# Kernel optimization log

Hardware: AMD Instinct MI355X
Metric: run time of the kernel (lower is better)

## Reference

```python
import jax, jax.numpy as jnp
import numpy as np

HID = 1024   # hidden_size
HEADS = 16   # multi_head
DH = 64      # hidden_size_head
FF = 4096    # ff_size
EPS = 1e-6   # LayerNorm epsilon
NEG = -1e9


def setup_inputs() -> dict:
    key = jax.random.key(0)
    ks = jax.random.split(key, 24)
    B, LI, LQ, LK = 16, 512, 64, 128
    s = 0.02

    def w(k, shape):
        return jax.random.normal(k, shape, jnp.float32) * s

    return {
        "img_feat": jax.random.normal(ks[0], (B, LI, HID), jnp.float32),
        "ques": jax.random.normal(ks[1], (B, LQ, HID), jnp.float32),
        "kg": jax.random.normal(ks[2], (B, LK, HID), jnp.float32),
        "ques_mask": jax.random.randint(ks[3], (B, LQ), 0, 2, jnp.int32),
        "kg_mask": jax.random.randint(ks[4], (B, LK), 0, 2, jnp.int32),
        # stacked params for the 3 MHAtt blocks; torch Linear weight layout [out, in]
        "att_qw": w(ks[5], (3, HID, HID)), "att_qb": jnp.zeros((3, HID), jnp.float32),
        "att_kw": w(ks[6], (3, HID, HID)), "att_kb": jnp.zeros((3, HID), jnp.float32),
        "att_vw": w(ks[7], (3, HID, HID)), "att_vb": jnp.zeros((3, HID), jnp.float32),
        "att_ow": w(ks[8], (3, HID, HID)), "att_ob": jnp.zeros((3, HID), jnp.float32),
        "ffn_w1": w(ks[9], (FF, HID)), "ffn_b1": jnp.zeros((FF,), jnp.float32),
        "ffn_w2": w(ks[10], (HID, FF)), "ffn_b2": jnp.zeros((HID,), jnp.float32),
        "ln_g": jnp.ones((4, HID), jnp.float32), "ln_b": jnp.zeros((4, HID), jnp.float32),
    }


def _ln(x, g, b):
    m = jnp.mean(x, axis=-1, keepdims=True)
    v = jnp.mean(jnp.square(x - m), axis=-1, keepdims=True)
    return g * (x - m) / jnp.sqrt(v + EPS) + b


def _mha(v_in, k_in, q_in, mask, qw, qb, kw, kb, vw, vb, ow, ob):
    B = q_in.shape[0]

    def proj(x, wt, bi):  # [B,S,H] -> [B,heads,S,DH]
        y = jnp.einsum('bsh,oh->bso', x, wt) + bi
        return y.reshape(B, -1, HEADS, DH).transpose(0, 2, 1, 3)

    q = proj(q_in, qw, qb)
    k = proj(k_in, kw, kb)
    v = proj(v_in, vw, vb)
    scores = jnp.einsum('bhqd,bhkd->bhqk', q, k) / jnp.sqrt(jnp.float32(DH))
    if mask is not None:
        scores = jnp.where(mask[:, None, None, :] == 1, NEG, scores)
    a = jax.nn.softmax(scores, axis=-1)  # dropout is identity at eval
    o = jnp.einsum('bhqk,bhkd->bhqd', a, v).transpose(0, 2, 1, 3).reshape(B, -1, HID)
    return jnp.einsum('bsh,oh->bso', o, ow) + ob


def reference(img_feat, ques, kg, ques_mask, kg_mask,
              att_qw, att_qb, att_kw, att_kb, att_vw, att_vb, att_ow, att_ob,
              ffn_w1, ffn_b1, ffn_w2, ffn_b2, ln_g, ln_b):
    x = img_feat
    # self-attention on image features (no mask)
    x = _ln(x + _mha(x, x, x, None,
                     att_qw[0], att_qb[0], att_kw[0], att_kb[0],
                     att_vw[0], att_vb[0], att_ow[0], att_ob[0]), ln_g[0], ln_b[0])
    # cross-attention to question
    x = _ln(x + _mha(ques, ques, x, ques_mask,
                     att_qw[1], att_qb[1], att_kw[1], att_kb[1],
                     att_vw[1], att_vb[1], att_ow[1], att_ob[1]), ln_g[1], ln_b[1])
    # cross-attention to knowledge graph facts
    x = _ln(x + _mha(kg, kg, x, kg_mask,
                     att_qw[2], att_qb[2], att_kw[2], att_kb[2],
                     att_vw[2], att_vb[2], att_ow[2], att_ob[2]), ln_g[2], ln_b[2])
    # FFN: Linear -> ReLU -> Linear (dropout identity at eval)
    h = jax.nn.relu(jnp.einsum('bsh,fh->bsf', x, ffn_w1) + ffn_b1)
    f = jnp.einsum('bsf,hf->bsh', h, ffn_w2) + ffn_b2
    x = _ln(x + f, ln_g[3], ln_b[3])
    return x
```

## Files before the change

kernel.cpp:

```cpp
#include <hip/hip_runtime.h>
#include <math.h>

#define HIDN 1024
#define NHEADS 16
#define DHEAD 64
#define FFD 4096
#define LN_EPS 1e-6f
#define NEGV -1e9f

typedef __bf16 bf16_t;
typedef __bf16 bf16x8 __attribute__((ext_vector_type(8)));
typedef float f32x4 __attribute__((ext_vector_type(4)));
typedef unsigned short ushort8 __attribute__((ext_vector_type(8)));
typedef unsigned short ushort4v __attribute__((ext_vector_type(4)));

__device__ __forceinline__ unsigned short f2bf(float f) {
    unsigned u = __float_as_uint(f);
    return (unsigned short)((u + 0x7FFFu + ((u >> 16) & 1u)) >> 16);
}
__device__ __forceinline__ float bf2f(unsigned short u) {
    return __uint_as_float((unsigned)u << 16);
}
__device__ __forceinline__ void gld16(const void* g, void* l) {
    __builtin_amdgcn_global_load_lds(
        (const __attribute__((address_space(1))) void*)g,
        (__attribute__((address_space(3))) void*)l, 16, 0, 0);
}

template<int RELU>
__global__ __launch_bounds__(256)
void gemm_mfma(const bf16_t* __restrict__ A, const bf16_t* __restrict__ W,
               const float* __restrict__ ba, const float* __restrict__ bb,
               const float* __restrict__ bc, const float* __restrict__ bd,
               unsigned short* __restrict__ Cb, int M, int N, int K)
{
    __shared__ __align__(16) bf16_t As[2][128 * 64];
    __shared__ __align__(16) bf16_t Bs[2][128 * 64];

    const int tid  = threadIdx.x;
    const int wid  = tid >> 6;
    const int lane = tid & 63;
    const int m0 = blockIdx.x * 128;
    const int n0 = blockIdx.y * 128;
    const int wm = (wid & 1) * 64;
    const int wn = (wid >> 1) * 64;

    const int sr = (wid << 3) + (lane >> 3);
    const int sk = (((lane & 7) ^ (lane >> 3)) * 8);
    const bf16_t* pa = A + (size_t)(m0 + sr) * K + sk;
    const bf16_t* pb = W + (size_t)(n0 + sr) * K + sk;
    const int lofs = (wid << 3) * 64;

    const int lr  = lane & 15;
    const int hi_ = lane >> 4;
    const int ch0 = ((hi_ + 0) ^ (lane & 7)) * 8;
    const int ch1 = ((hi_ + 4) ^ (lane & 7)) * 8;

    f32x4 acc[4][4];
    #pragma unroll
    for (int i = 0; i < 4; ++i)
        #pragma unroll
        for (int j = 0; j < 4; ++j) acc[i][j] = (f32x4){0.f, 0.f, 0.f, 0.f};

    auto stage = [&](int buf, int koff) {
        #pragma unroll
        for (int c = 0; c < 4; ++c) {
            gld16(pa + (size_t)c * 32 * K + koff, &As[buf][lofs + c * 32 * 64]);
            gld16(pb + (size_t)c * 32 * K + koff, &Bs[buf][lofs + c * 32 * 64]);
        }
    };
    auto compute = [&](int buf) {
        const bf16_t* fa = &As[buf][(wm + lr) * 64];
        const bf16_t* fb = &Bs[buf][(wn + lr) * 64];
        #pragma unroll
        for (int kk = 0; kk < 2; ++kk) {
            const int ch = kk ? ch1 : ch0;
            bf16x8 a[4], b[4];
            #pragma unroll
            for (int i = 0; i < 4; ++i) {
                a[i] = *(const bf16x8*)(fa + i * 16 * 64 + ch);
                b[i] = *(const bf16x8*)(fb + i * 16 * 64 + ch);
            }
            #pragma unroll
            for (int i = 0; i < 4; ++i)
                #pragma unroll
                for (int j = 0; j < 4; ++j)
                    acc[i][j] = __builtin_amdgcn_mfma_f32_16x16x32_bf16(
                        a[i], b[j], acc[i][j], 0, 0, 0);
        }
    };

    stage(0, 0);
    asm volatile("s_waitcnt vmcnt(0)" ::: "memory");
    __syncthreads();

    for (int k0 = 0; k0 < K; k0 += 128) {
        if (k0 + 64 < K) stage(1, k0 + 64);
        compute(0);
        asm volatile("s_waitcnt vmcnt(0)" ::: "memory");
        __syncthreads();
        if (k0 + 128 < K) stage(0, k0 + 128);
        compute(1);
        asm volatile("s_waitcnt vmcnt(0)" ::: "memory");
        __syncthreads();
    }

    const int seg = n0 >> 10;
    const float* bias = (seg == 0) ? ba : (seg == 1) ? bb : (seg == 2) ? bc : bd;
    const int nl = (n0 & 1023);
    const int er = wm + (lane >> 4) * 4;
    const int ec = wn + (lane & 15);
    float bv[4];
    #pragma unroll
    for (int j = 0; j < 4; ++j) bv[j] = bias[nl + ec + j * 16];
    #pragma unroll
    for (int i = 0; i < 4; ++i)
        #pragma unroll
        for (int j = 0; j < 4; ++j)
            #pragma unroll
            for (int r = 0; r < 4; ++r) {
                float v = acc[i][j][r] + bv[j];
                if (RELU) v = fmaxf(v, 0.f);
                Cb[(size_t)(m0 + er + i * 16 + r) * N + (n0 + ec + j * 16)] = f2bf(v);
            }
}

#define MFMA16(F0, F1, F2, F3)                                                      \
    acc[F0][0] = __builtin_amdgcn_mfma_f32_16x16x32_bf16(a0, b0, acc[F0][0], 0,0,0); \
    acc[F0][1] = __builtin_amdgcn_mfma_f32_16x16x32_bf16(a0, b1, acc[F0][1], 0,0,0); \
    acc[F0][2] = __builtin_amdgcn_mfma_f32_16x16x32_bf16(a0, b2, acc[F0][2], 0,0,0); \
    acc[F0][3] = __builtin_amdgcn_mfma_f32_16x16x32_bf16(a0, b3, acc[F0][3], 0,0,0); \
    acc[F1][0] = __builtin_amdgcn_mfma_f32_16x16x32_bf16(a1, b0, acc[F1][0], 0,0,0); \
    acc[F1][1] = __builtin_amdgcn_mfma_f32_16x16x32_bf16(a1, b1, acc[F1][1], 0,0,0); \
    acc[F1][2] = __builtin_amdgcn_mfma_f32_16x16x32_bf16(a1, b2, acc[F1][2], 0,0,0); \
    acc[F1][3] = __builtin_amdgcn_mfma_f32_16x16x32_bf16(a1, b3, acc[F1][3], 0,0,0); \
    acc[F2][0] = __builtin_amdgcn_mfma_f32_16x16x32_bf16(a2, b0, acc[F2][0], 0,0,0); \
    acc[F2][1] = __builtin_amdgcn_mfma_f32_16x16x32_bf16(a2, b1, acc[F2][1], 0,0,0); \
    acc[F2][2] = __builtin_amdgcn_mfma_f32_16x16x32_bf16(a2, b2, acc[F2][2], 0,0,0); \
    acc[F2][3] = __builtin_amdgcn_mfma_f32_16x16x32_bf16(a2, b3, acc[F2][3], 0,0,0); \
    acc[F3][0] = __builtin_amdgcn_mfma_f32_16x16x32_bf16(a3, b0, acc[F3][0], 0,0,0); \
    acc[F3][1] = __builtin_amdgcn_mfma_f32_16x16x32_bf16(a3, b1, acc[F3][1], 0,0,0); \
    acc[F3][2] = __builtin_amdgcn_mfma_f32_16x16x32_bf16(a3, b2, acc[F3][2], 0,0,0); \
    acc[F3][3] = __builtin_amdgcn_mfma_f32_16x16x32_bf16(a3, b3, acc[F3][3], 0,0,0);

#define PHASE_SYNC()                                           \
    __builtin_amdgcn_s_barrier();                              \
    asm volatile("s_waitcnt lgkmcnt(0)" ::: "memory");         \
    __builtin_amdgcn_sched_barrier(0);

template<int RELU>
__global__ __launch_bounds__(512, 1)
void gemm_mfma256(const bf16_t* __restrict__ A, const bf16_t* __restrict__ W,
                  const float* __restrict__ ba, const float* __restrict__ bb,
                  const float* __restrict__ bc, const float* __restrict__ bd,
                  unsigned short* __restrict__ Cb, int M, int N, int K)
{
    __shared__ __align__(16) bf16_t As[2][256 * 64];
    __shared__ __align__(16) bf16_t Bs[2][256 * 64];

    const int tid  = threadIdx.x;
    const int wid  = tid >> 6;
    const int lane = tid & 63;
    const int lo   = lane & 15;
    const int hi   = lane >> 4;

    const int GY = gridDim.y;
    const int id = blockIdx.y * gridDim.x + blockIdx.x;
    const int xcd = id & 7;
    const int c   = id >> 3;
    const int CN  = GY >> 1;
    const int m_idx = ((xcd & 3) << 3) + (c & 7);
    const int n_idx = (xcd >> 2) * CN + (c >> 3);
    const int m0 = m_idx * 256;
    const int n0 = n_idx * 256;

    const int wm = (wid & 1) * 128;
    const int wn = (wid >> 1) * 64;

    const int srow = tid >> 3;
    const int ssk  = (((tid & 7) ^ (srow & 7)) * 8);
    const bf16_t* pa = A + (size_t)(m0 + srow) * K + ssk;
    const bf16_t* pb = W + (size_t)(n0 + srow) * K + ssk;
    const int lbase = (wid << 3) * 64;

    auto stageA = [&](int buf, int koff) {
        #pragma unroll
        for (int i = 0; i < 4; ++i)
            gld16(pa + (size_t)i * 64 * K + koff, &As[buf][i * 64 * 64 + lbase]);
    };
    auto stageB = [&](int buf, int koff) {
        #pragma unroll
        for (int i = 0; i < 4; ++i)
            gld16(pb + (size_t)i * 64 * K + koff, &Bs[buf][i * 64 * 64 + lbase]);
    };

    auto ldA = [&](int buf, int f, int cc) -> bf16x8 {
        const int row = wm + f * 16 + lo;
        const int ch  = ((cc * 4 + hi) ^ (lo & 7)) * 8;
        return *(const bf16x8*)&As[buf][row * 64 + ch];
    };
    auto ldB = [&](int buf, int g, int cc) -> bf16x8 {
        const int row = wn + g * 16 + lo;
        const int ch  = ((cc * 4 + hi) ^ (lo & 7)) * 8;
        return *(const bf16x8*)&Bs[buf][row * 64 + ch];
    };

    f32x4 acc[8][4];
    #pragma unroll
    for (int f = 0; f < 8; ++f)
        #pragma unroll
        for (int g = 0; g < 4; ++g) acc[f][g] = (f32x4){0.f, 0.f, 0.f, 0.f};

    stageA(0, 0);
    stageB(0, 0);
    asm volatile("s_waitcnt vmcnt(0)" ::: "memory");
    __builtin_amdgcn_s_barrier();

    const int nt = K >> 6;
    for (int t = 0; t < nt; ++t) {
        const int buf = t & 1;
        const int knext = (t + 1) << 6;
        const bool pf = (t + 1 < nt);
        bf16x8 a0, a1, a2, a3, b0, b1, b2, b3;

        a0 = ldA(buf, 0, 0); a1 = ldA(buf, 1, 0); a2 = ldA(buf, 2, 0); a3 = ldA(buf, 3, 0);
        b0 = ldB(buf, 0, 0); b1 = ldB(buf, 1, 0); b2 = ldB(buf, 2, 0); b3 = ldB(buf, 3, 0);
        if (pf) stageA(buf ^ 1, knext);
        PHASE_SYNC();
        __builtin_amdgcn_s_setprio(1);
        MFMA16(0, 1, 2, 3);
        __builtin_amdgcn_s_setprio(0);
        __builtin_amdgcn_s_barrier();

        a0 = ldA(buf, 4, 0); a1 = ldA(buf, 5, 0); a2 = ldA(buf, 6, 0); a3 = ldA(buf, 7, 0);
        if (pf) stageB(buf ^ 1, knext);
        PHASE_SYNC();
        __builtin_amdgcn_s_setprio(1);
        MFMA16(4, 5, 6, 7);
        __builtin_amdgcn_s_setprio(0);
        __builtin_amdgcn_s_barrier();

        a0 = ldA(buf, 0, 1); a1 = ldA(buf, 1, 1); a2 = ldA(buf, 2, 1); a3 = ldA(buf, 3, 1);
        b0 = ldB(buf, 0, 1); b1 = ldB(buf, 1, 1); b2 = ldB(buf, 2, 1); b3 = ldB(buf, 3, 1);
        PHASE_SYNC();
        __builtin_amdgcn_s_setprio(1);
        MFMA16(0, 1, 2, 3);
        __builtin_amdgcn_s_setprio(0);
        __builtin_amdgcn_s_barrier();

        a0 = ldA(buf, 4, 1); a1 = ldA(buf, 5, 1); a2 = ldA(buf, 6, 1); a3 = ldA(buf, 7, 1);
        PHASE_SYNC();
        __builtin_amdgcn_s_setprio(1);
        MFMA16(4, 5, 6, 7);
        __builtin_amdgcn_s_setprio(0);
        asm volatile("s_waitcnt vmcnt(0)" ::: "memory");
        __builtin_amdgcn_s_barrier();
    }

    const int seg = n0 >> 10;
    const float* bias = (seg == 0) ? ba : (seg == 1) ? bb : (seg == 2) ? bc : bd;
    const int nl = (n0 & 1023);
    float bv[4];
    #pragma unroll
    for (int g = 0; g < 4; ++g) bv[g] = bias[nl + wn + g * 16 + lo];
    #pragma unroll
    for (int f = 0; f < 8; ++f)
        #pragma unroll
        for (int g = 0; g < 4; ++g)
            #pragma unroll
            for (int r = 0; r < 4; ++r) {
                float v = acc[f][g][r] + bv[g];
                if (RELU) v = fmaxf(v, 0.f);
                Cb[(size_t)(m0 + wm + f * 16 + hi * 4 + r) * N
                   + (n0 + wn + g * 16 + lo)] = f2bf(v);
            }
}

template<int HAS_MASK>
__global__ __launch_bounds__(512, 2)
void attn_mfma(const bf16_t* __restrict__ Q, const bf16_t* __restrict__ K,
               const bf16_t* __restrict__ V, int qstride, int kvstride,
               const int* __restrict__ mask,
               unsigned short* __restrict__ O, int Lk)
{
    __shared__ __align__(16) unsigned short Ks[64][72];
    __shared__ __align__(16) unsigned short Vt[64][72];
    __shared__ __align__(16) unsigned short Ps[128][72];
    __shared__ int smask[64];

    const int tid  = threadIdx.x;
    const int wid  = tid >> 6;
    const int lane = tid & 63;
    const int lo   = lane & 15;
    const int hi   = lane >> 4;
    const int h    = blockIdx.x;
    const int b    = blockIdx.y;
    const int Lq   = 512;

    bf16x8 qf[4][2];
    #pragma unroll
    for (int s4 = 0; s4 < 4; ++s4) {
        const bf16_t* qp = Q + (size_t)(b*Lq + s4*128 + wid*16 + lo) * qstride
                             + h*DHEAD + hi*8;
        qf[s4][0] = *(const bf16x8*)qp;
        qf[s4][1] = *(const bf16x8*)(qp + 32);
    }

    float mrun[4][4], lrun[4][4];
    f32x4 Oc[4][4];
    #pragma unroll
    for (int s4 = 0; s4 < 4; ++s4)
        #pragma unroll
        for (int r = 0; r < 4; ++r) {
            mrun[s4][r] = -INFINITY; lrun[s4][r] = 0.f;
            Oc[s4][r] = (f32x4){0.f, 0.f, 0.f, 0.f};
        }

    ushort8 r0, r1;
    int mreg = 0;

    auto load_tile = [&](int k0) {
        if (tid < 256) {
            const int sr = tid >> 2, sc = (tid & 3) * 16;
            const unsigned short* kp = (const unsigned short*)
                (K + (size_t)(b*Lk + k0 + sr) * kvstride + h*DHEAD + sc);
            r0 = *(const ushort8*)kp;
            r1 = *(const ushort8*)(kp + 8);
        } else {
            const int t2 = tid - 256, sr = t2 >> 2, sc = (t2 & 3) * 16;
            const unsigned short* vp = (const unsigned short*)
                (V + (size_t)(b*Lk + k0 + sr) * kvstride + h*DHEAD + sc);
            r0 = *(const ushort8*)vp;
            r1 = *(const ushort8*)(vp + 8);
        }
        if (HAS_MASK && tid < 64) mreg = mask[b*Lk + k0 + tid];
    };
    auto store_tile = [&]() {
        if (tid < 256) {
            const int sr = tid >> 2, sc = (tid & 3) * 16;
            const int x = ((sr >> 3) & 7) << 3;
            *(ushort8*)&Ks[sr][sc ^ x]       = r0;
            *(ushort8*)&Ks[sr][(sc + 8) ^ x] = r1;
        } else {
            const int t2 = tid - 256, sr = t2 >> 2, sc = (t2 & 3) * 16;
            #pragma unroll
            for (int t = 0; t < 8; ++t) {
                const int d0 = sc + t, d1 = sc + 8 + t;
                Vt[d0][sr ^ (((d0 >> 3) & 7) << 3)] = r0[t];
                Vt[d1][sr ^ (((d1 >> 3) & 7) << 3)] = r1[t];
            }
        }
        if (HAS_MASK && tid < 64) smask[tid] = mreg;
    };

    load_tile(0);
    store_tile();
    __syncthreads();

    int k0 = 0;
    while (true) {
        const bool more = (k0 + 64 < Lk);
        if (more) load_tile(k0 + 64);

        #pragma unroll
        for (int s4 = 0; s4 < 4; ++s4) {
            f32x4 sv[4];
            #pragma unroll
            for (int j = 0; j < 4; ++j) sv[j] = (f32x4){0.f, 0.f, 0.f, 0.f};
            #pragma unroll
            for (int kk = 0; kk < 2; ++kk) {
                #pragma unroll
                for (int j = 0; j < 4; ++j) {
                    const int krow = j*16 + lo;
                    const int kcol = (kk*32 + hi*8) ^ (((krow >> 3) & 7) << 3);
                    bf16x8 bfrag = *(const bf16x8*)&Ks[krow][kcol];
                    sv[j] = __builtin_amdgcn_mfma_f32_16x16x32_bf16(
                        qf[s4][kk], bfrag, sv[j], 0, 0, 0);
                }
            }
            #pragma unroll
            for (int j = 0; j < 4; ++j) {
                bool msk = HAS_MASK ? (smask[j*16 + lo] != 0) : false;
                #pragma unroll
                for (int r = 0; r < 4; ++r) {
                    float x = sv[j][r] * 0.125f;
                    sv[j][r] = msk ? NEGV : x;
                }
            }
            #pragma unroll
            for (int r = 0; r < 4; ++r) {
                float tm = fmaxf(fmaxf(sv[0][r], sv[1][r]), fmaxf(sv[2][r], sv[3][r]));
                #pragma unroll
                for (int m = 1; m < 16; m <<= 1) tm = fmaxf(tm, __shfl_xor(tm, m));
                float mnew = fmaxf(mrun[s4][r], tm);
                float f = __expf(mrun[s4][r] - mnew);
                float ps = 0.f;
                #pragma unroll
                for (int j = 0; j < 4; ++j) {
                    float p = __expf(sv[j][r] - mnew);
                    sv[j][r] = p;
                    ps += p;
                }
                #pragma unroll
                for (int m = 1; m < 16; m <<= 1) ps += __shfl_xor(ps, m);
                lrun[s4][r] = lrun[s4][r] * f + ps;
                mrun[s4][r] = mnew;
                #pragma unroll
                for (int n = 0; n < 4; ++n) Oc[s4][n][r] *= f;
                #pragma unroll
                for (int j = 0; j < 4; ++j)
                    Ps[wid*16 + hi*4 + r][j*16 + lo] = f2bf(sv[j][r]);
            }
            #pragma unroll
            for (int kk = 0; kk < 2; ++kk) {
                bf16x8 pa = *(const bf16x8*)&Ps[wid*16 + lo][kk*32 + hi*8];
                #pragma unroll
                for (int n = 0; n < 4; ++n) {
                    const int vrow = n*16 + lo;
                    const int vcol = (kk*32 + hi*8) ^ (((vrow >> 3) & 7) << 3);
                    bf16x8 vf = *(const bf16x8*)&Vt[vrow][vcol];
                    Oc[s4][n] = __builtin_amdgcn_mfma_f32_16x16x32_bf16(
                        pa, vf, Oc[s4][n], 0, 0, 0);
                }
            }
        }

        if (!more) break;
        __syncthreads();
        store_tile();
        __syncthreads();
        k0 += 64;
    }

    #pragma unroll
    for (int s4 = 0; s4 < 4; ++s4)
        #pragma unroll
        for (int r = 0; r < 4; ++r) {
            float inv = 1.f / lrun[s4][r];
            const size_t row = (size_t)(b*Lq + s4*128 + wid*16 + hi*4 + r) * HIDN
                             + h*DHEAD;
            #pragma unroll
            for (int n = 0; n < 4; ++n)
                O[row + n*16 + lo] = f2bf(Oc[s4][n][r] * inv);
        }
}

template<int WF32, int WBF>
__global__ __launch_bounds__(256)
void ln_res_b(const unsigned short* __restrict__ X, const unsigned short* __restrict__ R,
              const float* __restrict__ G, const float* __restrict__ Bv,
              unsigned short* __restrict__ OutB, float* __restrict__ OutF)
{
    const int row = blockIdx.x;
    const int tid = threadIdx.x;
    const size_t base = (size_t)row * HIDN + tid * 4;
    ushort4v xv = *(const ushort4v*)(X + base);
    ushort4v rv = *(const ushort4v*)(R + base);
    float y[4];
    #pragma unroll
    for (int t = 0; t < 4; ++t) y[t] = bf2f(xv[t]) + bf2f(rv[t]);
    float s1 = y[0] + y[1] + y[2] + y[3];
    float s2 = y[0]*y[0] + y[1]*y[1] + y[2]*y[2] + y[3]*y[3];
    #pragma unroll
    for (int m = 1; m < 64; m <<= 1) {
        s1 += __shfl_xor(s1, m);
        s2 += __shfl_xor(s2, m);
    }
    __shared__ float red1[4], red2[4];
    const int wave = tid >> 6, lane = tid & 63;
    if (lane == 0) { red1[wave] = s1; red2[wave] = s2; }
    __syncthreads();
    s1 = red1[0] + red1[1] + red1[2] + red1[3];
    s2 = red2[0] + red2[1] + red2[2] + red2[3];
    const float mean = s1 * (1.f / HIDN);
    const float var  = s2 * (1.f / HIDN) - mean * mean;
    const float inv  = rsqrtf(var + LN_EPS);
    float4 gv = *(const float4*)(G + tid*4);
    float4 bv = *(const float4*)(Bv + tid*4);
    float o[4];
    o[0] = gv.x * (y[0]-mean) * inv + bv.x;
    o[1] = gv.y * (y[1]-mean) * inv + bv.y;
    o[2] = gv.z * (y[2]-mean) * inv + bv.z;
    o[3] = gv.w * (y[3]-mean) * inv + bv.w;
    if (WBF) {
        ushort4v ob;
        #pragma unroll
        for (int t = 0; t < 4; ++t) ob[t] = f2bf(o[t]);
        *(ushort4v*)(OutB + base) = ob;
    }
    if (WF32) {
        float4 of = {o[0], o[1], o[2], o[3]};
        *(float4*)(OutF + base) = of;
    }
}

struct CvtArgs {
    const float* src[32];
    unsigned short* dst[32];
};

__global__ __launch_bounds__(256)
void cvt_units(CvtArgs args)
{
    const float* s = args.src[blockIdx.y];
    unsigned short* d = args.dst[blockIdx.y];
    const int i = blockIdx.x * 256 + threadIdx.x;
    const float4* p = (const float4*)s + (size_t)i * 2;
    float4 a = p[0], b = p[1];
    ushort8 o;
    o[0] = f2bf(a.x); o[1] = f2bf(a.y); o[2] = f2bf(a.z); o[3] = f2bf(a.w);
    o[4] = f2bf(b.x); o[5] = f2bf(b.y); o[6] = f2bf(b.z); o[7] = f2bf(b.w);
    ((ushort8*)d)[i] = o;
}

extern "C" void kernel_launch(void* const* d_in, const int* in_sizes, int n_in,
                              void* d_out, int out_size, void* d_ws, size_t ws_size,
                              hipStream_t stream)
{
    const float* img   = (const float*)d_in[0];
    const float* ques  = (const float*)d_in[1];
    const float* kg    = (const float*)d_in[2];
    const int*   qmask = (const int*)d_in[3];
    const int*   kmask = (const int*)d_in[4];
    const float* qw = (const float*)d_in[5];
    const float* qb = (const float*)d_in[6];
    const float* kw = (const float*)d_in[7];
    const float* kb = (const float*)d_in[8];
    const float* vw = (const float*)d_in[9];
    const float* vb = (const float*)d_in[10];
    const float* ow = (const float*)d_in[11];
    const float* ob = (const float*)d_in[12];
    const float* w1 = (const float*)d_in[13];
    const float* b1 = (const float*)d_in[14];
    const float* w2 = (const float*)d_in[15];
    const float* b2 = (const float*)d_in[16];
    const float* lng = (const float*)d_in[17];
    const float* lnb = (const float*)d_in[18];
    float* out = (float*)d_out;

    const int B = 16;
    const int NX = B * 512;
    const size_t WSTEP = (size_t)1024 * 1024;
    const size_t MB = (size_t)1 << 20;
    const size_t MELEM = (size_t)1024 * 1024;

    char* wsb = (char*)d_ws;
    unsigned short* xb    = (unsigned short*)(wsb);
    unsigned short* bM    = (unsigned short*)(wsb + 16*MB);
    unsigned short* bOb   = (unsigned short*)(wsb + 32*MB);
    unsigned short* quesb = (unsigned short*)(wsb + 48*MB);
    unsigned short* kgb   = (unsigned short*)(wsb + 50*MB);
    unsigned short* wa    = (unsigned short*)(wsb + 56*MB);
    unsigned short* bQKV  = (unsigned short*)(wsb + 96*MB);
    unsigned short* bKV   = (unsigned short*)(wsb + 144*MB);
    unsigned short* hb    = (unsigned short*)(wsb + 96*MB);

    CvtArgs ca;
    int u = 0;
    auto addu = [&](const float* src, int melems, unsigned short* dst) {
        for (int i = 0; i < melems; ++i) {
            ca.src[u] = src + (size_t)i * MELEM;
            ca.dst[u] = dst + (size_t)i * MELEM;
            ++u;
        }
    };
    addu(qw + 0*WSTEP, 1, wa + 0*MELEM);
    addu(kw + 0*WSTEP, 1, wa + 1*MELEM);
    addu(vw + 0*WSTEP, 1, wa + 2*MELEM);
    addu(qw + 1*WSTEP, 1, wa + 3*MELEM);
    addu(kw + 1*WSTEP, 1, wa + 4*MELEM);
    addu(vw + 1*WSTEP, 1, wa + 5*MELEM);
    addu(qw + 2*WSTEP, 1, wa + 6*MELEM);
    addu(kw + 2*WSTEP, 1, wa + 7*MELEM);
    addu(vw + 2*WSTEP, 1, wa + 8*MELEM);
    addu(ow + 0*WSTEP, 1, wa + 9*MELEM);
    addu(ow + 1*WSTEP, 1, wa + 10*MELEM);
    addu(ow + 2*WSTEP, 1, wa + 11*MELEM);
    addu(w1, 4, wa + 12*MELEM);
    addu(w2, 4, wa + 16*MELEM);
    addu(img,  8, xb);
    addu(ques, 1, quesb);
    addu(kg,   2, kgb);

    dim3 blk(256);
    cvt_units<<<dim3(512, u), blk, 0, stream>>>(ca);

    auto gemm = [&](const unsigned short* A, const unsigned short* W,
                    const float* ba, const float* bb_, const float* bc, const float* bd,
                    unsigned short* C, int M, int N, int K, int relu) {
        if (N >= 3072 && (M % 256) == 0 && (N % 256) == 0
            && ((M / 256) % 8) == 0 && ((N / 256) % 2) == 0) {
            dim3 grid(M / 256, N / 256);
            if (relu) gemm_mfma256<1><<<grid, dim3(512), 0, stream>>>(
                (const bf16_t*)A, (const bf16_t*)W, ba, bb_, bc, bd, C, M, N, K);
            else      gemm_mfma256<0><<<grid, dim3(512), 0, stream>>>(
                (const bf16_t*)A, (const bf16_t*)W, ba, bb_, bc, bd, C, M, N, K);
            return;
        }
        dim3 grid(M / 128, N / 128);
        if (relu) gemm_mfma<1><<<grid, blk, 0, stream>>>(
            (const bf16_t*)A, (const bf16_t*)W, ba, bb_, bc, bd, C, M, N, K);
        else      gemm_mfma<0><<<grid, blk, 0, stream>>>(
            (const bf16_t*)A, (const bf16_t*)W, ba, bb_, bc, bd, C, M, N, K);
    };

    const unsigned short* Akv[3] = {xb, quesb, kgb};
    const int Mkv[3] = {NX, B * 64, B * 128};
    const int Lk[3]  = {512, 64, 128};

    dim3 ablk(512);
    dim3 agrid(NHEADS, B);

    for (int t = 0; t < 3; ++t) {
        if (t == 0) {
            gemm(xb, wa + 0*MELEM, qb + 0, kb + 0, vb + 0, vb + 0,
                 bQKV, NX, 3072, 1024, 0);
            attn_mfma<0><<<agrid, ablk, 0, stream>>>(
                (const bf16_t*)bQKV, (const bf16_t*)bQKV + 1024, (const bf16_t*)bQKV + 2048,
                3072, 3072, nullptr, bOb, Lk[t]);
        } else {
            gemm(xb, wa + (t == 1 ? 3 : 6)*MELEM,
                 qb + t*1024, qb + t*1024, qb + t*1024, qb + t*1024,
                 bQKV, NX, 1024, 1024, 0);
            gemm(Akv[t], wa + (t == 1 ? 4 : 7)*MELEM,
                 kb + t*1024, vb + t*1024, vb + t*1024, vb + t*1024,
                 bKV, Mkv[t], 2048, 1024, 0);
            attn_mfma<1><<<agrid, ablk, 0, stream>>>(
                (const bf16_t*)bQKV, (const bf16_t*)bKV, (const bf16_t*)bKV + 1024,
                1024, 2048, (t == 1 ? qmask : kmask), bOb, Lk[t]);
        }
        gemm(bOb, wa + (9 + t)*MELEM,
             ob + t*1024, ob + t*1024, ob + t*1024, ob + t*1024,
             bM, NX, 1024, 1024, 0);
        ln_res_b<0,1><<<NX, blk, 0, stream>>>(xb, bM, lng + t*1024, lnb + t*1024, xb, nullptr);
    }

    gemm(xb, wa + 12*MELEM, b1, b1 + 1024, b1 + 2048, b1 + 3072, hb, NX, FFD, 1024, 1);
    gemm(hb, wa + 16*MELEM, b2, b2, b2, b2, bM, NX, 1024, 4096, 0);
    ln_res_b<1,0><<<NX, blk, 0, stream>>>(xb, bM, lng + 3*1024, lnb + 3*1024, nullptr, out);
}
```

Before: 516.5 us.

## Simplify 256-tile GEMM main loop to plain double-buffered stage/compute

Replaces the hand-scheduled four-phase ping-pong loop of the 256x256 GEMM (barriers between sub-phases, split A/B prefetch, s_setprio around MFMA bursts) with a simpler loop. Each K-step issues a combined A+B prefetch into the other buffer, loads all A/B fragments, runs 32 MFMAs per half-tile, then waits and synchronises once. The aim is to cut barrier overhead and let the compiler schedule LDS reads and MFMAs freely. The cost is losing the explicit interleaving and priority hints, and holding more fragment registers live at once. Dispatch now also requires K to be a multiple of 128.

```diff
diff --git a/kernel.cpp b/kernel.cpp
--- a/kernel.cpp
+++ b/kernel.cpp
@@ -125,29 +125,6 @@
             }
 }
 
-#define MFMA16(F0, F1, F2, F3)                                                      \
-    acc[F0][0] = __builtin_amdgcn_mfma_f32_16x16x32_bf16(a0, b0, acc[F0][0], 0,0,0); \
-    acc[F0][1] = __builtin_amdgcn_mfma_f32_16x16x32_bf16(a0, b1, acc[F0][1], 0,0,0); \
-    acc[F0][2] = __builtin_amdgcn_mfma_f32_16x16x32_bf16(a0, b2, acc[F0][2], 0,0,0); \
-    acc[F0][3] = __builtin_amdgcn_mfma_f32_16x16x32_bf16(a0, b3, acc[F0][3], 0,0,0); \
-    acc[F1][0] = __builtin_amdgcn_mfma_f32_16x16x32_bf16(a1, b0, acc[F1][0], 0,0,0); \
-    acc[F1][1] = __builtin_amdgcn_mfma_f32_16x16x32_bf16(a1, b1, acc[F1][1], 0,0,0); \
-    acc[F1][2] = __builtin_amdgcn_mfma_f32_16x16x32_bf16(a1, b2, acc[F1][2], 0,0,0); \
-    acc[F1][3] = __builtin_amdgcn_mfma_f32_16x16x32_bf16(a1, b3, acc[F1][3], 0,0,0); \
-    acc[F2][0] = __builtin_amdgcn_mfma_f32_16x16x32_bf16(a2, b0, acc[F2][0], 0,0,0); \
-    acc[F2][1] = __builtin_amdgcn_mfma_f32_16x16x32_bf16(a2, b1, acc[F2][1], 0,0,0); \
-    acc[F2][2] = __builtin_amdgcn_mfma_f32_16x16x32_bf16(a2, b2, acc[F2][2], 0,0,0); \
-    acc[F2][3] = __builtin_amdgcn_mfma_f32_16x16x32_bf16(a2, b3, acc[F2][3], 0,0,0); \
-    acc[F3][0] = __builtin_amdgcn_mfma_f32_16x16x32_bf16(a3, b0, acc[F3][0], 0,0,0); \
-    acc[F3][1] = __builtin_amdgcn_mfma_f32_16x16x32_bf16(a3, b1, acc[F3][1], 0,0,0); \
-    acc[F3][2] = __builtin_amdgcn_mfma_f32_16x16x32_bf16(a3, b2, acc[F3][2], 0,0,0); \
-    acc[F3][3] = __builtin_amdgcn_mfma_f32_16x16x32_bf16(a3, b3, acc[F3][3], 0,0,0);
-
-#define PHASE_SYNC()                                           \
-    __builtin_amdgcn_s_barrier();                              \
-    asm volatile("s_waitcnt lgkmcnt(0)" ::: "memory");         \
-    __builtin_amdgcn_sched_barrier(0);
-
 template<int RELU>
 __global__ __launch_bounds__(512, 1)
 void gemm_mfma256(const bf16_t* __restrict__ A, const bf16_t* __restrict__ W,
@@ -183,26 +160,12 @@
     const bf16_t* pb = W + (size_t)(n0 + srow) * K + ssk;
     const int lbase = (wid << 3) * 64;
 
-    auto stageA = [&](int buf, int koff) {
-        #pragma unroll
-        for (int i = 0; i < 4; ++i)
+    auto stage = [&](int buf, int koff) {
+        #pragma unroll
+        for (int i = 0; i < 4; ++i) {
             gld16(pa + (size_t)i * 64 * K + koff, &As[buf][i * 64 * 64 + lbase]);
-    };
-    auto stageB = [&](int buf, int koff) {
-        #pragma unroll
-        for (int i = 0; i < 4; ++i)
             gld16(pb + (size_t)i * 64 * K + koff, &Bs[buf][i * 64 * 64 + lbase]);
-    };
-
-    auto ldA = [&](int buf, int f, int cc) -> bf16x8 {
-        const int row = wm + f * 16 + lo;
-        const int ch  = ((cc * 4 + hi) ^ (lo & 7)) * 8;
-        return *(const bf16x8*)&As[buf][row * 64 + ch];
-    };
-    auto ldB = [&](int buf, int g, int cc) -> bf16x8 {
-        const int row = wn + g * 16 + lo;
-        const int ch  = ((cc * 4 + hi) ^ (lo & 7)) * 8;
-        return *(const bf16x8*)&Bs[buf][row * 64 + ch];
+        }
     };
 
     f32x4 acc[8][4];
@@ -211,50 +174,44 @@
         #pragma unroll
         for (int g = 0; g < 4; ++g) acc[f][g] = (f32x4){0.f, 0.f, 0.f, 0.f};
 
-    stageA(0, 0);
-    stageB(0, 0);
+    auto compute = [&](int buf) {
+        #pragma unroll
+        for (int kk = 0; kk < 2; ++kk) {
+            bf16x8 a[8], b[4];
+            #pragma unroll
+            for (int f = 0; f < 8; ++f) {
+                const int row = wm + f * 16 + lo;
+                const int ch  = ((kk * 4 + hi) ^ (lo & 7)) * 8;
+                a[f] = *(const bf16x8*)&As[buf][row * 64 + ch];
+            }
+            #pragma unroll
+            for (int g = 0; g < 4; ++g) {
+                const int row = wn + g * 16 + lo;
+                const int ch  = ((kk * 4 + hi) ^ (lo & 7)) * 8;
+                b[g] = *(const bf16x8*)&Bs[buf][row * 64 + ch];
+            }
+            #pragma unroll
+            for (int f = 0; f < 8; ++f)
+                #pragma unroll
+                for (int g = 0; g < 4; ++g)
+                    acc[f][g] = __builtin_amdgcn_mfma_f32_16x16x32_bf16(
+                        a[f], b[g], acc[f][g], 0, 0, 0);
+        }
+    };
+
+    stage(0, 0);
     asm volatile("s_waitcnt vmcnt(0)" ::: "memory");
-    __builtin_amdgcn_s_barrier();
-
-    const int nt = K >> 6;
-    for (int t = 0; t < nt; ++t) {
-        const int buf = t & 1;
-        const int knext = (t + 1) << 6;
-        const bool pf = (t + 1 < nt);
-        bf16x8 a0, a1, a2, a3, b0, b1, b2, b3;
-
-        a0 = ldA(buf, 0, 0); a1 = ldA(buf, 1, 0); a2 = ldA(buf, 2, 0); a3 = ldA(buf, 3, 0);
-        b0 = ldB(buf, 0, 0); b1 = ldB(buf, 1, 0); b2 = ldB(buf, 2, 0); b3 = ldB(buf, 3, 0);
-        if (pf) stageA(buf ^ 1, knext);
-        PHASE_SYNC();
-        __builtin_amdgcn_s_setprio(1);
-        MFMA16(0, 1, 2, 3);
-        __builtin_amdgcn_s_setprio(0);
-        __builtin_amdgcn_s_barrier();
-
-        a0 = ldA(buf, 4, 0); a1 = ldA(buf, 5, 0); a2 = ldA(buf, 6, 0); a3 = ldA(buf, 7, 0);
-        if (pf) stageB(buf ^ 1, knext);
-        PHASE_SYNC();
-        __builtin_amdgcn_s_setprio(1);
-        MFMA16(4, 5, 6, 7);
-        __builtin_amdgcn_s_setprio(0);
-        __builtin_amdgcn_s_barrier();
-
-        a0 = ldA(buf, 0, 1); a1 = ldA(buf, 1, 1); a2 = ldA(buf, 2, 1); a3 = ldA(buf, 3, 1);
-        b0 = ldB(buf, 0, 1); b1 = ldB(buf, 1, 1); b2 = ldB(buf, 2, 1); b3 = ldB(buf, 3, 1);
-        PHASE_SYNC();
-        __builtin_amdgcn_s_setprio(1);
-        MFMA16(0, 1, 2, 3);
-        __builtin_amdgcn_s_setprio(0);
-        __builtin_amdgcn_s_barrier();
-
-        a0 = ldA(buf, 4, 1); a1 = ldA(buf, 5, 1); a2 = ldA(buf, 6, 1); a3 = ldA(buf, 7, 1);
-        PHASE_SYNC();
-        __builtin_amdgcn_s_setprio(1);
-        MFMA16(4, 5, 6, 7);
-        __builtin_amdgcn_s_setprio(0);
+    __syncthreads();
+
+    for (int k0 = 0; k0 < K; k0 += 128) {
+        if (k0 + 64 < K) stage(1, k0 + 64);
+        compute(0);
         asm volatile("s_waitcnt vmcnt(0)" ::: "memory");
-        __builtin_amdgcn_s_barrier();
+        __syncthreads();
+        if (k0 + 128 < K) stage(0, k0 + 128);
+        compute(1);
+        asm volatile("s_waitcnt vmcnt(0)" ::: "memory");
+        __syncthreads();
     }
 
     const int seg = n0 >> 10;
@@ -589,7 +546,7 @@
                     const float* ba, const float* bb_, const float* bc, const float* bd,
                     unsigned short* C, int M, int N, int K, int relu) {
         if (N >= 3072 && (M % 256) == 0 && (N % 256) == 0
-            && ((M / 256) % 8) == 0 && ((N / 256) % 2) == 0) {
+            && ((M / 256) % 8) == 0 && ((N / 256) % 2) == 0 && (K % 128) == 0) {
             dim3 grid(M / 256, N / 256);
             if (relu) gemm_mfma256<1><<<grid, dim3(512), 0, stream>>>(
                 (const bf16_t*)A, (const bf16_t*)W, ba, bb_, bc, bd, C, M, N, K);
```

New measurement: 513.5 us. About the same (-0.6%).

## Unroll GEMM K-loop by two and issue A-tile prefetch one step earlier

Applied to the files above, without the earlier changes.

Restructures the 256x256 MFMA GEMM main loop into a two-tile unrolled body. The A tile for the next-but-one step is staged right after the current tile's compute, and B is staged at the start of the next tile, with partial vmcnt waits replacing full drains. The aim is to keep more global loads in flight and overlap them with MFMA work instead of waiting on every load each iteration. The dispatch condition now requires M==8192 and K divisible by 128, which narrows when the fast path is used.

```diff
diff --git a/kernel.cpp b/kernel.cpp
--- a/kernel.cpp
+++ b/kernel.cpp
@@ -143,10 +143,20 @@
     acc[F3][2] = __builtin_amdgcn_mfma_f32_16x16x32_bf16(a3, b2, acc[F3][2], 0,0,0); \
     acc[F3][3] = __builtin_amdgcn_mfma_f32_16x16x32_bf16(a3, b3, acc[F3][3], 0,0,0);
 
-#define PHASE_SYNC()                                           \
-    __builtin_amdgcn_s_barrier();                              \
-    asm volatile("s_waitcnt lgkmcnt(0)" ::: "memory");         \
-    __builtin_amdgcn_sched_barrier(0);
+#define READ_A(BUF, FB, CC)                                      \
+    a0 = ldAf(BUF, (FB)+0, CC); a1 = ldAf(BUF, (FB)+1, CC);       \
+    a2 = ldAf(BUF, (FB)+2, CC); a3 = ldAf(BUF, (FB)+3, CC);
+#define READ_B(BUF, CC)                                          \
+    b0 = ldBf(BUF, 0, CC); b1 = ldBf(BUF, 1, CC);                 \
+    b2 = ldBf(BUF, 2, CC); b3 = ldBf(BUF, 3, CC);
+#define PHASE_MID()                                              \
+    __builtin_amdgcn_s_barrier();                                \
+    asm volatile("s_waitcnt lgkmcnt(0)" ::: "memory");           \
+    __builtin_amdgcn_sched_barrier(0);                           \
+    __builtin_amdgcn_s_setprio(1);
+#define PHASE_END()                                              \
+    __builtin_amdgcn_s_setprio(0);                               \
+    __builtin_amdgcn_s_barrier();
 
 template<int RELU>
 __global__ __launch_bounds__(512, 1)
@@ -169,10 +179,8 @@
     const int xcd = id & 7;
     const int c   = id >> 3;
     const int CN  = GY >> 1;
-    const int m_idx = ((xcd & 3) << 3) + (c & 7);
-    const int n_idx = (xcd >> 2) * CN + (c >> 3);
-    const int m0 = m_idx * 256;
-    const int n0 = n_idx * 256;
+    const int m0 = (((xcd & 3) << 3) + (c & 7)) * 256;
+    const int n0 = ((xcd >> 2) * CN + (c >> 3)) * 256;
 
     const int wm = (wid & 1) * 128;
     const int wn = (wid >> 1) * 64;
@@ -193,13 +201,12 @@
         for (int i = 0; i < 4; ++i)
             gld16(pb + (size_t)i * 64 * K + koff, &Bs[buf][i * 64 * 64 + lbase]);
     };
-
-    auto ldA = [&](int buf, int f, int cc) -> bf16x8 {
+    auto ldAf = [&](int buf, int f, int cc) -> bf16x8 {
         const int row = wm + f * 16 + lo;
         const int ch  = ((cc * 4 + hi) ^ (lo & 7)) * 8;
         return *(const bf16x8*)&As[buf][row * 64 + ch];
     };
-    auto ldB = [&](int buf, int g, int cc) -> bf16x8 {
+    auto ldBf = [&](int buf, int g, int cc) -> bf16x8 {
         const int row = wn + g * 16 + lo;
         const int ch  = ((cc * 4 + hi) ^ (lo & 7)) * 8;
         return *(const bf16x8*)&Bs[buf][row * 64 + ch];
@@ -211,49 +218,50 @@
         #pragma unroll
         for (int g = 0; g < 4; ++g) acc[f][g] = (f32x4){0.f, 0.f, 0.f, 0.f};
 
+    const int nt = K >> 6;
+
     stageA(0, 0);
     stageB(0, 0);
-    asm volatile("s_waitcnt vmcnt(0)" ::: "memory");
+    stageA(1, 64);
+    asm volatile("s_waitcnt vmcnt(4)" ::: "memory");
     __builtin_amdgcn_s_barrier();
 
-    const int nt = K >> 6;
-    for (int t = 0; t < nt; ++t) {
-        const int buf = t & 1;
-        const int knext = (t + 1) << 6;
-        const bool pf = (t + 1 < nt);
+    for (int t = 0; t < nt; t += 2) {
         bf16x8 a0, a1, a2, a3, b0, b1, b2, b3;
-
-        a0 = ldA(buf, 0, 0); a1 = ldA(buf, 1, 0); a2 = ldA(buf, 2, 0); a3 = ldA(buf, 3, 0);
-        b0 = ldB(buf, 0, 0); b1 = ldB(buf, 1, 0); b2 = ldB(buf, 2, 0); b3 = ldB(buf, 3, 0);
-        if (pf) stageA(buf ^ 1, knext);
-        PHASE_SYNC();
-        __builtin_amdgcn_s_setprio(1);
-        MFMA16(0, 1, 2, 3);
-        __builtin_amdgcn_s_setprio(0);
+        const int kB1 = (t + 1) << 6;
+
+        READ_A(0, 0, 0); READ_B(0, 0);
+        stageB(1, kB1);
+        PHASE_MID(); MFMA16(0, 1, 2, 3); PHASE_END();
+        READ_A(0, 4, 0);
+        PHASE_MID(); MFMA16(4, 5, 6, 7); PHASE_END();
+        READ_A(0, 0, 1); READ_B(0, 1);
+        PHASE_MID(); MFMA16(0, 1, 2, 3); PHASE_END();
+        READ_A(0, 4, 1);
+        PHASE_MID(); MFMA16(4, 5, 6, 7); PHASE_END();
+        if (t + 2 < nt) {
+            stageA(0, (t + 2) << 6);
+            asm volatile("s_waitcnt vmcnt(4)" ::: "memory");
+        } else {
+            asm volatile("s_waitcnt vmcnt(0)" ::: "memory");
+        }
         __builtin_amdgcn_s_barrier();
 
-        a0 = ldA(buf, 4, 0); a1 = ldA(buf, 5, 0); a2 = ldA(buf, 6, 0); a3 = ldA(buf, 7, 0);
-        if (pf) stageB(buf ^ 1, knext);
-        PHASE_SYNC();
-        __builtin_amdgcn_s_setprio(1);
-        MFMA16(4, 5, 6, 7);
-        __builtin_amdgcn_s_setprio(0);
-        __builtin_amdgcn_s_barrier();
-
-        a0 = ldA(buf, 0, 1); a1 = ldA(buf, 1, 1); a2 = ldA(buf, 2, 1); a3 = ldA(buf, 3, 1);
-        b0 = ldB(buf, 0, 1); b1 = ldB(buf, 1, 1); b2 = ldB(buf, 2, 1); b3 = ldB(buf, 3, 1);
-        PHASE_SYNC();
-        __builtin_amdgcn_s_setprio(1);
-        MFMA16(0, 1, 2, 3);
-        __builtin_amdgcn_s_setprio(0);
-        __builtin_amdgcn_s_barrier();
-
-        a0 = ldA(buf, 4, 1); a1 = ldA(buf, 5, 1); a2 = ldA(buf, 6, 1); a3 = ldA(buf, 7, 1);
-        PHASE_SYNC();
-        __builtin_amdgcn_s_setprio(1);
-        MFMA16(4, 5, 6, 7);
-        __builtin_amdgcn_s_setprio(0);
-        asm volatile("s_waitcnt vmcnt(0)" ::: "memory");
+        READ_A(1, 0, 0); READ_B(1, 0);
+        if (t + 2 < nt) stageB(0, (t + 2) << 6);
+        PHASE_MID(); MFMA16(0, 1, 2, 3); PHASE_END();
+        READ_A(1, 4, 0);
+        PHASE_MID(); MFMA16(4, 5, 6, 7); PHASE_END();
+        READ_A(1, 0, 1); READ_B(1, 1);
+        PHASE_MID(); MFMA16(0, 1, 2, 3); PHASE_END();
+        READ_A(1, 4, 1);
+        PHASE_MID(); MFMA16(4, 5, 6, 7); PHASE_END();
+        if (t + 3 < nt) {
+            stageA(1, (t + 3) << 6);
+            asm volatile("s_waitcnt vmcnt(4)" ::: "memory");
+        } else {
+            asm volatile("s_waitcnt vmcnt(0)" ::: "memory");
+        }
         __builtin_amdgcn_s_barrier();
     }
 
@@ -588,8 +596,8 @@
     auto gemm = [&](const unsigned short* A, const unsigned short* W,
                     const float* ba, const float* bb_, const float* bc, const float* bd,
                     unsigned short* C, int M, int N, int K, int relu) {
-        if (N >= 3072 && (M % 256) == 0 && (N % 256) == 0
-            && ((M / 256) % 8) == 0 && ((N / 256) % 2) == 0) {
+        if (N >= 3072 && M == 8192 && (N % 256) == 0
+            && ((N / 256) % 2) == 0 && (K % 128) == 0) {
             dim3 grid(M / 256, N / 256);
             if (relu) gemm_mfma256<1><<<grid, dim3(512), 0, stream>>>(
                 (const bf16_t*)A, (const bf16_t*)W, ba, bb_, bc, bd, C, M, N, K);
```

New measurement: 519.3 us. About the same (+0.5%).
